# Kernel optimization log

Hardware: AMD Instinct MI355X
Metric: run time of the kernel (lower is better)

The kernel has to match this reference:

```python
import jax, jax.numpy as jnp
import numpy as np

N_NODES = 50000
N_EDGES = 800000
IN_CH, HID_CH, OUT_CH = 512, 512, 256


def setup_inputs() -> dict:
    key = jax.random.key(0)
    ks = jax.random.split(key, 8)
    x = jax.random.normal(ks[0], (N_NODES, IN_CH), dtype=jnp.float32)
    edge_index = jax.random.randint(ks[1], (2, N_EDGES), 0, N_NODES, dtype=jnp.int32)
    def glorot(k, fan_in, fan_out):
        s = jnp.sqrt(6.0 / (fan_in + fan_out))
        return jax.random.uniform(k, (fan_in, fan_out), jnp.float32, -s, s)
    W1 = glorot(ks[2], IN_CH, HID_CH)
    b1 = jnp.zeros((HID_CH,), jnp.float32)
    W2 = glorot(ks[3], HID_CH, HID_CH)
    b2 = jnp.zeros((HID_CH,), jnp.float32)
    W3 = glorot(ks[4], HID_CH, OUT_CH)
    b3 = jnp.zeros((OUT_CH,), jnp.float32)
    return {"x": x, "edge_index": edge_index, "W1": W1, "b1": b1,
            "W2": W2, "b2": b2, "W3": W3, "b3": b3}


def _gcn_conv(x, src, dst, W, b, n_nodes):
    """PyG GCNConv: add self-loops, symmetric deg^-1/2 normalization,
    linear transform, scatter-add aggregation, bias."""
    h = x @ W  # [N, out] dense transform first (in >= out)
    # degree counts include the self-loop (+1)
    deg = jax.ops.segment_sum(jnp.ones(src.shape, x.dtype), dst,
                              num_segments=n_nodes) + 1.0
    dinv = jax.lax.rsqrt(deg)  # [N]
    norm = dinv[src] * dinv[dst]  # [E]
    msg = h[src] * norm[:, None]  # [E, out]
    agg = jax.ops.segment_sum(msg, dst, num_segments=n_nodes)
    # self-loop contribution handled analytically: norm_ii = dinv[i]^2
    return agg + h * (dinv * dinv)[:, None] + b


def reference(x, edge_index, W1, b1, W2, b2, W3, b3):
    src, dst = edge_index[0], edge_index[1]
    n = x.shape[0]
    h = _gcn_conv(x, src, dst, W1, b1, n)
    h = jax.nn.gelu(h)  # dropout p=0.0 -> identity
    h = _gcn_conv(h, src, dst, W2, b2, n)
    h = jax.nn.gelu(h)
    out = _gcn_conv(h, src, dst, W3, b3, n)
    return out
```

## Files before the change

### kernel.cpp

```cpp
#include <hip/hip_runtime.h>
#include <hip/hip_fp16.h>
#include <math.h>

#define N_NODES 50000
#define N_EDGES 800000
#define MPAD 50048
#define KPHYS 1024
#define KVIRT 1536
#define NKITER (KVIRT / 32)
#define SCANB ((N_NODES + 255) / 256)


__device__ __forceinline__ unsigned short bf16_rn(float f) {
    unsigned u = __float_as_uint(f);
    u += 0x7FFFu + ((u >> 16) & 1u);
    return (unsigned short)(u >> 16);
}
__device__ __forceinline__ float bf16_f32(unsigned short h) {
    return __uint_as_float(((unsigned)h) << 16);
}


typedef __attribute__((ext_vector_type(4))) float f4v;
typedef __attribute__((ext_vector_type(2))) float f2v;

__device__ __forceinline__ float4 ntload4(const float* p) {
    f4v v = __builtin_nontemporal_load((const f4v*)p);
    return make_float4(v[0], v[1], v[2], v[3]);
}
__device__ __forceinline__ float2 ntload2(const float* p) {
    f2v v = __builtin_nontemporal_load((const f2v*)p);
    return make_float2(v[0], v[1]);
}


__global__ void zero_int_kernel(int* __restrict__ p, int n) {
    int i = blockIdx.x * blockDim.x + threadIdx.x;
    if (i < n) p[i] = 0;
}

__global__ void count_deg_kernel(const int* __restrict__ dst, int* __restrict__ deg) {
    int e = blockIdx.x * blockDim.x + threadIdx.x;
    if (e < N_EDGES) atomicAdd(&deg[dst[e]], 1);
}

__global__ void dinv_kernel(const int* __restrict__ deg, float* __restrict__ dinv) {
    int i = blockIdx.x * blockDim.x + threadIdx.x;
    if (i < N_NODES) dinv[i] = rsqrtf((float)deg[i] + 1.0f);
}

__global__ __launch_bounds__(256) void scan1_kernel(const int* __restrict__ deg,
                                                    int* __restrict__ local_scan,
                                                    int* __restrict__ partials) {
    __shared__ int sm[256];
    int b = blockIdx.x, t = threadIdx.x;
    int i = b * 256 + t;
    int v = (i < N_NODES) ? deg[i] : 0;
    sm[t] = v;
    __syncthreads();
    for (int off = 1; off < 256; off <<= 1) {
        int x = (t >= off) ? sm[t - off] : 0;
        __syncthreads();
        sm[t] += x;
        __syncthreads();
    }
    if (i < N_NODES) local_scan[i] = sm[t];
    if (t == 255) partials[b] = sm[255];
}

__global__ __launch_bounds__(256) void scan2_kernel(int* __restrict__ partials) {
    __shared__ int sm[256];
    int t = threadIdx.x;
    sm[t] = (t < SCANB) ? partials[t] : 0;
    __syncthreads();
    for (int off = 1; off < 256; off <<= 1) {
        int x = (t >= off) ? sm[t - off] : 0;
        __syncthreads();
        sm[t] += x;
        __syncthreads();
    }
    if (t < SCANB) partials[t] = (t == 0) ? 0 : sm[t - 1];
}

__global__ __launch_bounds__(256) void scan3_kernel(const int* __restrict__ deg,
                                                    const int* __restrict__ local_scan,
                                                    const int* __restrict__ partials,
                                                    int* __restrict__ offsets,
                                                    int* __restrict__ cursor) {
    int i = blockIdx.x * 256 + threadIdx.x;
    if (i == 0) offsets[0] = 0;
    if (i < N_NODES) {
        int incl = local_scan[i] + partials[blockIdx.x];
        offsets[i + 1] = incl;
        cursor[i] = incl - deg[i];
    }
}

__global__ void fill_csr_kernel(const int* __restrict__ src, const int* __restrict__ dst,
                                int* __restrict__ cursor, int* __restrict__ csr_src,
                                float* __restrict__ csr_w, const float* __restrict__ dinv) {
    int e = blockIdx.x * blockDim.x + threadIdx.x;
    if (e < N_EDGES) {
        int s = src[e], d = dst[e];
        int p = atomicAdd(&cursor[d], 1);
        csr_src[p] = s;
        csr_w[p] = dinv[s] * dinv[d];
    }
}


typedef __attribute__((ext_vector_type(8))) short bf16x8;
typedef __attribute__((ext_vector_type(4))) float floatx4;

#define GLL16(g, l)                                                                   \
    __builtin_amdgcn_global_load_lds((__attribute__((address_space(1))) const void*)(g), \
                                     (__attribute__((address_space(3))) void*)(l), 16, 0, 0)

__global__ __launch_bounds__(256) void gemm_split_bt(const unsigned short* __restrict__ A2,
                                                     const unsigned short* __restrict__ B2T,
                                                     float* __restrict__ C,
                                                     __half* __restrict__ C16, int N) {
    __shared__ unsigned short As[2][128 * 32];
    __shared__ unsigned short Bs[2][128 * 32];

    const int t = threadIdx.x;
    const int lane = t & 63;
    const int quad = lane >> 4;
    const int l15 = lane & 15;
    const int w = t >> 6;
    const int wm = w & 1, wn = w >> 1;
    const int row0 = blockIdx.y * 128;
    const int col0 = blockIdx.x * 128;

    floatx4 acc[4][4];
#pragma unroll
    for (int i = 0; i < 4; i++)
#pragma unroll
        for (int j = 0; j < 4; j++) acc[i][j] = (floatx4){0.f, 0.f, 0.f, 0.f};

    const int sr = t >> 2;
    const int sk = ((t & 3) ^ ((t >> 3) & 3)) * 8;
    const unsigned short* Arow0 = A2 + (size_t)(row0 + sr) * KPHYS + sk;
    const unsigned short* Arow1 = Arow0 + (size_t)64 * KPHYS;
    const unsigned short* Brow0 = B2T + (size_t)(col0 + sr) * KVIRT + sk;
    const unsigned short* Brow1 = Brow0 + (size_t)64 * KVIRT;

    const int fcol = (quad ^ ((l15 >> 1) & 3)) * 8;

    {
        GLL16(Arow0 + 0, As[0] + t * 8);
        GLL16(Arow1 + 0, As[0] + 2048 + t * 8);
        GLL16(Brow0 + 0, Bs[0] + t * 8);
        GLL16(Brow1 + 0, Bs[0] + 2048 + t * 8);
    }

    for (int it = 0; it < NKITER; it++) {
        const int cur = it & 1;
        __syncthreads();
        if (it + 1 < NKITER) {
            const int kbn = (it + 1) * 32;
            const int kAn = (kbn < KPHYS) ? kbn : kbn - KPHYS;
            const int nxt = cur ^ 1;
            GLL16(Arow0 + kAn, As[nxt] + t * 8);
            GLL16(Arow1 + kAn, As[nxt] + 2048 + t * 8);
            GLL16(Brow0 + kbn, Bs[nxt] + t * 8);
            GLL16(Brow1 + kbn, Bs[nxt] + 2048 + t * 8);
        }

        bf16x8 af[4], bf[4];
#pragma unroll
        for (int mt = 0; mt < 4; mt++)
            af[mt] = *(const bf16x8*)(As[cur] + (wm * 64 + mt * 16 + l15) * 32 + fcol);
#pragma unroll
        for (int nt = 0; nt < 4; nt++)
            bf[nt] = *(const bf16x8*)(Bs[cur] + (wn * 64 + nt * 16 + l15) * 32 + fcol);
#pragma unroll
        for (int mt = 0; mt < 4; mt++)
#pragma unroll
            for (int nt = 0; nt < 4; nt++)
                acc[mt][nt] = __builtin_amdgcn_mfma_f32_16x16x32_bf16(af[mt], bf[nt], acc[mt][nt], 0, 0, 0);
    }

#pragma unroll
    for (int mt = 0; mt < 4; mt++) {
#pragma unroll
        for (int r = 0; r < 4; r++) {
            int row = row0 + wm * 64 + mt * 16 + quad * 4 + r;
            float* Cp = C + (size_t)row * N + col0 + wn * 64 + l15;
            __half* Cp16 = C16 + (size_t)row * N + col0 + wn * 64 + l15;
#pragma unroll
            for (int nt = 0; nt < 4; nt++) {
                __builtin_nontemporal_store(acc[mt][nt][r], Cp + nt * 16);
                Cp16[nt * 16] = __float2half(acc[mt][nt][r]);
            }
        }
    }
}


__global__ void wsplit_kernel(const float* __restrict__ W, unsigned short* __restrict__ B2T, int N) {
    int idx = blockIdx.x * blockDim.x + threadIdx.x;
    if (idx >= 512 * N) return;
    int k = idx / N, n = idx % N;
    float v = W[(size_t)k * N + n];
    unsigned short hi = bf16_rn(v);
    unsigned short lo = bf16_rn(v - bf16_f32(hi));
    unsigned short* row = B2T + (size_t)n * KVIRT;
    row[k] = hi;
    row[512 + k] = hi;
    row[1024 + k] = lo;
}


__global__ __launch_bounds__(256) void split_x_kernel(const float* __restrict__ x,
                                                      unsigned short* __restrict__ A2) {
    int m = blockIdx.x;
    int ch = threadIdx.x * 2;
    unsigned short* arow = A2 + (size_t)m * KPHYS;
    float vx = 0.f, vy = 0.f;
    if (m < N_NODES) {
        float2 v = ntload2(x + (size_t)m * 512 + ch);
        vx = v.x;
        vy = v.y;
    }
    unsigned short hx = bf16_rn(vx), hy = bf16_rn(vy);
    arow[ch] = hx;
    arow[ch + 1] = hy;
    arow[512 + ch] = bf16_rn(vx - bf16_f32(hx));
    arow[512 + ch + 1] = bf16_rn(vy - bf16_f32(hy));
}


__device__ __forceinline__ float gelu_tanh(float x) {
    float x3 = x * x * x;
    float inner = 0.7978845608028654f * (x + 0.044715f * x3);
    return 0.5f * x * (1.0f + tanhf(inner));
}

__global__ __launch_bounds__(256) void aggregate_split_kernel(
    const float* __restrict__ h32, const __half* __restrict__ h16,
    const int* __restrict__ offsets, const int* __restrict__ csr_src,
    const float* __restrict__ csr_w, const float* __restrict__ dinv,
    const float* __restrict__ bias, unsigned short* __restrict__ A2) {
    int t = threadIdx.x;
    int node = __builtin_amdgcn_readfirstlane(blockIdx.x * 4 + (t >> 6));
    int ch = (t & 63) * 8;
    unsigned short* arow = A2 + (size_t)node * KPHYS;
    if (node >= N_NODES) {
        *(uint4*)(arow + ch) = make_uint4(0, 0, 0, 0);
        *(uint4*)(arow + 512 + ch) = make_uint4(0, 0, 0, 0);
        return;
    }
    int p0 = offsets[node], p1 = offsets[node + 1];
    float a[8] = {0.f, 0.f, 0.f, 0.f, 0.f, 0.f, 0.f, 0.f};

    union H8 { float4 f4; __half2 h2[4]; };
    int p = p0;
    int pend4 = p0 + ((p1 - p0) & ~3);
    for (; p < pend4; p += 4) {
        int s0 = csr_src[p], s1 = csr_src[p + 1], s2 = csr_src[p + 2], s3 = csr_src[p + 3];
        float w0 = csr_w[p], w1 = csr_w[p + 1], w2 = csr_w[p + 2], w3 = csr_w[p + 3];
        H8 v0, v1, v2, v3;
        v0.f4 = *(const float4*)(h16 + (size_t)s0 * 512 + ch);
        v1.f4 = *(const float4*)(h16 + (size_t)s1 * 512 + ch);
        v2.f4 = *(const float4*)(h16 + (size_t)s2 * 512 + ch);
        v3.f4 = *(const float4*)(h16 + (size_t)s3 * 512 + ch);
#pragma unroll
        for (int j = 0; j < 4; j++) {
            float2 c0 = __half22float2(v0.h2[j]);
            float2 c1 = __half22float2(v1.h2[j]);
            float2 c2 = __half22float2(v2.h2[j]);
            float2 c3 = __half22float2(v3.h2[j]);
            a[2 * j] += w0 * c0.x + w1 * c1.x + w2 * c2.x + w3 * c3.x;
            a[2 * j + 1] += w0 * c0.y + w1 * c1.y + w2 * c2.y + w3 * c3.y;
        }
    }
    for (; p < p1; p++) {
        int s = csr_src[p];
        float wg = csr_w[p];
        H8 v;
        v.f4 = *(const float4*)(h16 + (size_t)s * 512 + ch);
#pragma unroll
        for (int j = 0; j < 4; j++) {
            float2 c = __half22float2(v.h2[j]);
            a[2 * j] += wg * c.x;
            a[2 * j + 1] += wg * c.y;
        }
    }

    float di = dinv[node];
    float wself = di * di;
    float4 hs0 = ntload4(h32 + (size_t)node * 512 + ch);
    float4 hs1 = ntload4(h32 + (size_t)node * 512 + ch + 4);
    float4 bv0 = *(const float4*)(bias + ch);
    float4 bv1 = *(const float4*)(bias + ch + 4);
    float s[8] = {hs0.x, hs0.y, hs0.z, hs0.w, hs1.x, hs1.y, hs1.z, hs1.w};
    float b[8] = {bv0.x, bv0.y, bv0.z, bv0.w, bv1.x, bv1.y, bv1.z, bv1.w};

    unsigned short hi[8], lo[8];
#pragma unroll
    for (int j = 0; j < 8; j++) {
        float v = gelu_tanh(a[j] + wself * s[j] + b[j]);
        hi[j] = bf16_rn(v);
        lo[j] = bf16_rn(v - bf16_f32(hi[j]));
    }
    *(ushort4*)(arow + ch) = make_ushort4(hi[0], hi[1], hi[2], hi[3]);
    *(ushort4*)(arow + ch + 4) = make_ushort4(hi[4], hi[5], hi[6], hi[7]);
    *(ushort4*)(arow + 512 + ch) = make_ushort4(lo[0], lo[1], lo[2], lo[3]);
    *(ushort4*)(arow + 512 + ch + 4) = make_ushort4(lo[4], lo[5], lo[6], lo[7]);
}

__global__ __launch_bounds__(256) void aggregate_final_kernel(
    const float* __restrict__ h32, const __half* __restrict__ h16,
    const int* __restrict__ offsets, const int* __restrict__ csr_src,
    const float* __restrict__ csr_w, const float* __restrict__ dinv,
    const float* __restrict__ bias, float* __restrict__ out) {
    int t = threadIdx.x;
    int node = __builtin_amdgcn_readfirstlane(blockIdx.x * 4 + (t >> 6));
    if (node >= N_NODES) return;
    int ch = (t & 63) * 4;
    int p0 = offsets[node], p1 = offsets[node + 1];
    float ax = 0.f, ay = 0.f, az = 0.f, aw = 0.f;

    union H4 { float2 f2; __half2 h2[2]; };
    int p = p0;
    int pend4 = p0 + ((p1 - p0) & ~3);
    for (; p < pend4; p += 4) {
        int s0 = csr_src[p], s1 = csr_src[p + 1], s2 = csr_src[p + 2], s3 = csr_src[p + 3];
        float w0 = csr_w[p], w1 = csr_w[p + 1], w2 = csr_w[p + 2], w3 = csr_w[p + 3];
        H4 v0, v1, v2, v3;
        v0.f2 = *(const float2*)(h16 + (size_t)s0 * 256 + ch);
        v1.f2 = *(const float2*)(h16 + (size_t)s1 * 256 + ch);
        v2.f2 = *(const float2*)(h16 + (size_t)s2 * 256 + ch);
        v3.f2 = *(const float2*)(h16 + (size_t)s3 * 256 + ch);
        float2 c00 = __half22float2(v0.h2[0]), c01 = __half22float2(v0.h2[1]);
        float2 c10 = __half22float2(v1.h2[0]), c11 = __half22float2(v1.h2[1]);
        float2 c20 = __half22float2(v2.h2[0]), c21 = __half22float2(v2.h2[1]);
        float2 c30 = __half22float2(v3.h2[0]), c31 = __half22float2(v3.h2[1]);
        ax += w0 * c00.x + w1 * c10.x + w2 * c20.x + w3 * c30.x;
        ay += w0 * c00.y + w1 * c10.y + w2 * c20.y + w3 * c30.y;
        az += w0 * c01.x + w1 * c11.x + w2 * c21.x + w3 * c31.x;
        aw += w0 * c01.y + w1 * c11.y + w2 * c21.y + w3 * c31.y;
    }
    for (; p < p1; p++) {
        int s = csr_src[p];
        float wg = csr_w[p];
        H4 v;
        v.f2 = *(const float2*)(h16 + (size_t)s * 256 + ch);
        float2 c0 = __half22float2(v.h2[0]), c1 = __half22float2(v.h2[1]);
        ax += wg * c0.x; ay += wg * c0.y; az += wg * c1.x; aw += wg * c1.y;
    }

    float di = dinv[node];
    float wself = di * di;
    float4 hs = ntload4(h32 + (size_t)node * 256 + ch);
    float4 bv = *(const float4*)(bias + ch);
    float4 o = make_float4(ax + wself * hs.x + bv.x, ay + wself * hs.y + bv.y,
                           az + wself * hs.z + bv.z, aw + wself * hs.w + bv.w);
    *(float4*)(out + (size_t)node * 256 + ch) = o;
}


static inline char* align16(char* p) { return (char*)(((size_t)p + 15) & ~(size_t)15); }

extern "C" void kernel_launch(void* const* d_in, const int* in_sizes, int n_in,
                              void* d_out, int out_size, void* d_ws, size_t ws_size,
                              hipStream_t stream) {
    const float* x  = (const float*)d_in[0];
    const int* eidx = (const int*)d_in[1];
    const float* W1 = (const float*)d_in[2];
    const float* b1 = (const float*)d_in[3];
    const float* W2 = (const float*)d_in[4];
    const float* b2 = (const float*)d_in[5];
    const float* W3 = (const float*)d_in[6];
    const float* b3 = (const float*)d_in[7];
    float* out = (float*)d_out;

    const int* src = eidx;
    const int* dst = eidx + N_EDGES;

    char* ws = (char*)d_ws;
    unsigned short* A2 = (unsigned short*)ws;  ws += (size_t)MPAD * KPHYS * 2;
    float* Cbuf = (float*)ws;                  ws += (size_t)MPAD * 512 * 4;
    __half* C16 = (__half*)ws;                 ws += (size_t)MPAD * 512 * 2;
    unsigned short* B2T1 = (unsigned short*)ws; ws += (size_t)512 * KVIRT * 2;
    unsigned short* B2T2 = (unsigned short*)ws; ws += (size_t)512 * KVIRT * 2;
    unsigned short* B2T3 = (unsigned short*)ws; ws += (size_t)256 * KVIRT * 2;
    int* deg = (int*)ws;        ws = align16(ws + (size_t)N_NODES * 4);
    float* dinv = (float*)ws;   ws = align16(ws + (size_t)N_NODES * 4);
    int* offsets = (int*)ws;    ws = align16(ws + (size_t)(N_NODES + 1) * 4);
    int* cursor = (int*)ws;     ws = align16(ws + (size_t)N_NODES * 4);
    int* csr_src = (int*)ws;    ws = align16(ws + (size_t)N_EDGES * 4);
    float* csr_w = (float*)ws;  ws = align16(ws + (size_t)N_EDGES * 4);
    int* local_scan = (int*)ws; ws = align16(ws + (size_t)N_NODES * 4);
    int* partials = (int*)ws;   ws = align16(ws + (size_t)SCANB * 4);

    zero_int_kernel<<<(N_NODES + 255) / 256, 256, 0, stream>>>(deg, N_NODES);
    count_deg_kernel<<<(N_EDGES + 255) / 256, 256, 0, stream>>>(dst, deg);
    dinv_kernel<<<(N_NODES + 255) / 256, 256, 0, stream>>>(deg, dinv);
    scan1_kernel<<<SCANB, 256, 0, stream>>>(deg, local_scan, partials);
    scan2_kernel<<<1, 256, 0, stream>>>(partials);
    scan3_kernel<<<SCANB, 256, 0, stream>>>(deg, local_scan, partials, offsets, cursor);
    fill_csr_kernel<<<(N_EDGES + 255) / 256, 256, 0, stream>>>(src, dst, cursor, csr_src, csr_w, dinv);

    wsplit_kernel<<<(512 * 512 + 255) / 256, 256, 0, stream>>>(W1, B2T1, 512);
    wsplit_kernel<<<(512 * 512 + 255) / 256, 256, 0, stream>>>(W2, B2T2, 512);
    wsplit_kernel<<<(512 * 256 + 255) / 256, 256, 0, stream>>>(W3, B2T3, 256);
    split_x_kernel<<<MPAD, 256, 0, stream>>>(x, A2);

    {
        dim3 grid(512 / 128, MPAD / 128);
        gemm_split_bt<<<grid, 256, 0, stream>>>(A2, B2T1, Cbuf, C16, 512);
        aggregate_split_kernel<<<MPAD / 4, 256, 0, stream>>>(Cbuf, C16, offsets, csr_src, csr_w, dinv, b1, A2);
    }
    {
        dim3 grid(512 / 128, MPAD / 128);
        gemm_split_bt<<<grid, 256, 0, stream>>>(A2, B2T2, Cbuf, C16, 512);
        aggregate_split_kernel<<<MPAD / 4, 256, 0, stream>>>(Cbuf, C16, offsets, csr_src, csr_w, dinv, b2, A2);
    }
    {
        dim3 grid(256 / 128, MPAD / 128);
        gemm_split_bt<<<grid, 256, 0, stream>>>(A2, B2T3, Cbuf, C16, 256);
        aggregate_final_kernel<<<MPAD / 4, 256, 0, stream>>>(Cbuf, C16, offsets, csr_src, csr_w, dinv, b3, out);
    }
}
```

Before: 1.002 ms.

## Reuse hi/lo bf16 fragments across three split-precision MFMA passes per k-step

The split-bf16 GEMM no longer uses a virtual K of 1536 that reloads the A hi/lo halves. Each outer step now stages the A hi, A lo, B hi and B lo tiles together and issues three MFMA passes (hi*hi, lo*hi, hi*lo) from registers. The B weight buffer shrinks to K=1024 with no duplicated hi copy. This cuts global and LDS traffic for A and B and halves the number of barriers. In exchange it doubles LDS use per block and raises register pressure, which may lower occupancy.

```diff
diff --git a/kernel.cpp b/kernel.cpp
--- a/kernel.cpp
+++ b/kernel.cpp
@@ -6,8 +6,8 @@
 #define N_EDGES 800000
 #define MPAD 50048
 #define KPHYS 1024
-#define KVIRT 1536
-#define NKITER (KVIRT / 32)
+#define KB 1024
+#define NOUTER 16
 #define SCANB ((N_NODES + 255) / 256)
 
 
@@ -120,8 +120,8 @@
                                                      const unsigned short* __restrict__ B2T,
                                                      float* __restrict__ C,
                                                      __half* __restrict__ C16, int N) {
-    __shared__ unsigned short As[2][128 * 32];
-    __shared__ unsigned short Bs[2][128 * 32];
+    __shared__ unsigned short As[2][2][128 * 32];
+    __shared__ unsigned short Bs[2][2][128 * 32];
 
     const int t = threadIdx.x;
     const int lane = t & 63;
@@ -142,44 +142,60 @@
     const int sk = ((t & 3) ^ ((t >> 3) & 3)) * 8;
     const unsigned short* Arow0 = A2 + (size_t)(row0 + sr) * KPHYS + sk;
     const unsigned short* Arow1 = Arow0 + (size_t)64 * KPHYS;
-    const unsigned short* Brow0 = B2T + (size_t)(col0 + sr) * KVIRT + sk;
-    const unsigned short* Brow1 = Brow0 + (size_t)64 * KVIRT;
+    const unsigned short* Brow0 = B2T + (size_t)(col0 + sr) * KB + sk;
+    const unsigned short* Brow1 = Brow0 + (size_t)64 * KB;
 
     const int fcol = (quad ^ ((l15 >> 1) & 3)) * 8;
 
-    {
-        GLL16(Arow0 + 0, As[0] + t * 8);
-        GLL16(Arow1 + 0, As[0] + 2048 + t * 8);
-        GLL16(Brow0 + 0, Bs[0] + t * 8);
-        GLL16(Brow1 + 0, Bs[0] + 2048 + t * 8);
-    }
-
-    for (int it = 0; it < NKITER; it++) {
+#define STAGE(buf, k32)                                            \
+    do {                                                           \
+        GLL16(Arow0 + (k32), As[buf][0] + t * 8);                  \
+        GLL16(Arow1 + (k32), As[buf][0] + 2048 + t * 8);           \
+        GLL16(Arow0 + 512 + (k32), As[buf][1] + t * 8);            \
+        GLL16(Arow1 + 512 + (k32), As[buf][1] + 2048 + t * 8);     \
+        GLL16(Brow0 + (k32), Bs[buf][0] + t * 8);                  \
+        GLL16(Brow1 + (k32), Bs[buf][0] + 2048 + t * 8);           \
+        GLL16(Brow0 + 512 + (k32), Bs[buf][1] + t * 8);            \
+        GLL16(Brow1 + 512 + (k32), Bs[buf][1] + 2048 + t * 8);     \
+    } while (0)
+
+    STAGE(0, 0);
+
+    for (int it = 0; it < NOUTER; it++) {
         const int cur = it & 1;
         __syncthreads();
-        if (it + 1 < NKITER) {
-            const int kbn = (it + 1) * 32;
-            const int kAn = (kbn < KPHYS) ? kbn : kbn - KPHYS;
-            const int nxt = cur ^ 1;
-            GLL16(Arow0 + kAn, As[nxt] + t * 8);
-            GLL16(Arow1 + kAn, As[nxt] + 2048 + t * 8);
-            GLL16(Brow0 + kbn, Bs[nxt] + t * 8);
-            GLL16(Brow1 + kbn, Bs[nxt] + 2048 + t * 8);
+        if (it + 1 < NOUTER) STAGE(cur ^ 1, (it + 1) * 32);
+
+        bf16x8 afh[4], afl[4], bfh[4], bfl[4];
+#pragma unroll
+        for (int mt = 0; mt < 4; mt++) {
+            const int ro = (wm * 64 + mt * 16 + l15) * 32 + fcol;
+            afh[mt] = *(const bf16x8*)(As[cur][0] + ro);
+            afl[mt] = *(const bf16x8*)(As[cur][1] + ro);
         }
-
-        bf16x8 af[4], bf[4];
+#pragma unroll
+        for (int nt = 0; nt < 4; nt++) {
+            const int ro = (wn * 64 + nt * 16 + l15) * 32 + fcol;
+            bfh[nt] = *(const bf16x8*)(Bs[cur][0] + ro);
+            bfl[nt] = *(const bf16x8*)(Bs[cur][1] + ro);
+        }
 #pragma unroll
         for (int mt = 0; mt < 4; mt++)
-            af[mt] = *(const bf16x8*)(As[cur] + (wm * 64 + mt * 16 + l15) * 32 + fcol);
-#pragma unroll
-        for (int nt = 0; nt < 4; nt++)
-            bf[nt] = *(const bf16x8*)(Bs[cur] + (wn * 64 + nt * 16 + l15) * 32 + fcol);
+#pragma unroll
+            for (int nt = 0; nt < 4; nt++)
+                acc[mt][nt] = __builtin_amdgcn_mfma_f32_16x16x32_bf16(afh[mt], bfh[nt], acc[mt][nt], 0, 0, 0);
 #pragma unroll
         for (int mt = 0; mt < 4; mt++)
 #pragma unroll
             for (int nt = 0; nt < 4; nt++)
-                acc[mt][nt] = __builtin_amdgcn_mfma_f32_16x16x32_bf16(af[mt], bf[nt], acc[mt][nt], 0, 0, 0);
-    }
+                acc[mt][nt] = __builtin_amdgcn_mfma_f32_16x16x32_bf16(afl[mt], bfh[nt], acc[mt][nt], 0, 0, 0);
+#pragma unroll
+        for (int mt = 0; mt < 4; mt++)
+#pragma unroll
+            for (int nt = 0; nt < 4; nt++)
+                acc[mt][nt] = __builtin_amdgcn_mfma_f32_16x16x32_bf16(afh[mt], bfl[nt], acc[mt][nt], 0, 0, 0);
+    }
+#undef STAGE
 
 #pragma unroll
     for (int mt = 0; mt < 4; mt++) {
@@ -205,10 +221,9 @@
     float v = W[(size_t)k * N + n];
     unsigned short hi = bf16_rn(v);
     unsigned short lo = bf16_rn(v - bf16_f32(hi));
-    unsigned short* row = B2T + (size_t)n * KVIRT;
+    unsigned short* row = B2T + (size_t)n * KB;
     row[k] = hi;
-    row[512 + k] = hi;
-    row[1024 + k] = lo;
+    row[512 + k] = lo;
 }
 
 
@@ -383,9 +398,9 @@
     unsigned short* A2 = (unsigned short*)ws;  ws += (size_t)MPAD * KPHYS * 2;
     float* Cbuf = (float*)ws;                  ws += (size_t)MPAD * 512 * 4;
     __half* C16 = (__half*)ws;                 ws += (size_t)MPAD * 512 * 2;
-    unsigned short* B2T1 = (unsigned short*)ws; ws += (size_t)512 * KVIRT * 2;
-    unsigned short* B2T2 = (unsigned short*)ws; ws += (size_t)512 * KVIRT * 2;
-    unsigned short* B2T3 = (unsigned short*)ws; ws += (size_t)256 * KVIRT * 2;
+    unsigned short* B2T1 = (unsigned short*)ws; ws += (size_t)512 * KB * 2;
+    unsigned short* B2T2 = (unsigned short*)ws; ws += (size_t)512 * KB * 2;
+    unsigned short* B2T3 = (unsigned short*)ws; ws += (size_t)256 * KB * 2;
     int* deg = (int*)ws;        ws = align16(ws + (size_t)N_NODES * 4);
     float* dinv = (float*)ws;   ws = align16(ws + (size_t)N_NODES * 4);
     int* offsets = (int*)ws;    ws = align16(ws + (size_t)(N_NODES + 1) * 4);
```

Result: faster. 923.9 us (-7.8%).
